# Performance work log

Hardware: AMD Instinct MI355X
Metric: run time of the kernel (lower is better)

Reference implementation:

```python
import jax, jax.numpy as jnp
import numpy as np

B, D, L = 16, 256, 200
T = 1000   # max_frame_length
K = 3      # kernel_size
DW, DC = 4, 2


def setup_inputs() -> dict:
    key = jax.random.key(0)
    ks = jax.random.split(key, 16)
    plen = jax.random.randint(ks[0], (B,), 150, L + 1)
    pm = jnp.arange(L)[None, :] < plen[:, None]              # (B,L) True=valid
    phoneme_mask = pm[:, None, :]                            # (B,1,L)
    durations = jax.random.uniform(ks[1], (B, L), minval=1.0, maxval=8.0) * pm
    phoneme = jax.random.normal(ks[2], (B, D, L), dtype=jnp.float32)
    s = 0.05
    params = {
        'Wpw': jax.random.normal(ks[3], (D, D)) * s, 'bpw': jnp.zeros((D,)),
        'Cw': jax.random.normal(ks[4], (8, D, K)) * s, 'cbw': jnp.zeros((8,)),
        'Mw': jax.random.normal(ks[5], (10, DW)) * s, 'mbw': jnp.zeros((DW,)),
        'Lw': jax.random.normal(ks[6], (DW * D, D)) * s, 'lbw': jnp.zeros((D,)),
        'Wpc': jax.random.normal(ks[7], (D, D)) * s, 'bpc': jnp.zeros((D,)),
        'Cc': jax.random.normal(ks[8], (8, D, K)) * s, 'cbc': jnp.zeros((8,)),
        'Mc': jax.random.normal(ks[9], (10, DC)) * s, 'mbc': jnp.zeros((DC,)),
        'Lc': jax.random.normal(ks[10], (DW * DC, D)) * s, 'lbc': jnp.zeros((D,)),
        'Wo': jax.random.normal(ks[11], (D, 2 * D)) * s, 'bo': jnp.zeros((2 * D,)),
    }
    return {'durations': durations, 'phoneme': phoneme, 'phoneme_mask': phoneme_mask, **params}


def _conv_swish(x, W1, b1, Ck, cb, pm):
    # 1x1 conv (proj) then kernel-K 'same' conv then SiLU; mask padded phones
    h = jnp.einsum('od,bdl->bol', W1, x) + b1[None, :, None]
    h = jax.lax.conv_general_dilated(h, Ck, (1,), 'SAME',
                                     dimension_numbers=('NCH', 'OIH', 'NCH')) + cb[None, :, None]
    h = jax.nn.silu(h)
    h = jnp.where(pm[:, None, :], h, 0.0)
    return h.transpose(0, 2, 1)  # (B, L, 8)


def _mlp(S, E, h, M, mb):
    # concat start/end boundary scalars with per-phone conv features -> (B,T,L,10)
    feat = jnp.concatenate([S[..., None], E[..., None],
                            jnp.broadcast_to(h[:, None], (B, T, L, 8))], axis=-1)
    return jax.nn.silu(feat @ M + mb)


def _forward(durations, phoneme, phoneme_mask, Wpw, bpw, Cw, cbw, Mw, mbw, Lw, lbw,
             Wpc, bpc, Cc, cbc, Mc, mbc, Lc, lbc, Wo, bo):
    pm = phoneme_mask[:, 0, :]                                          # (B,L)
    frame_lengths = jnp.clip(jnp.round(durations.sum(-1)).astype(jnp.int32), 0, T)
    frame_mask = jnp.arange(T)[None, :] < frame_lengths[:, None]        # (B,T)
    attn_mask = frame_mask[:, :, None] & pm[:, None, :]                 # (B,T,L)
    sd = jnp.cumsum(durations, axis=-1)                                 # (B,L)
    sk = sd - durations
    t = jnp.arange(1, T + 1, dtype=durations.dtype)
    S = jnp.where(attn_mask, t[None, :, None] - sk[:, None, :], 0.0)    # (B,T,L)
    E = jnp.where(attn_mask, (sd - sk)[:, None, :], 0.0)                # (B,T,L)

    h_w = _conv_swish(phoneme, Wpw, bpw, Cw, cbw, pm)
    w = _mlp(S, E, h_w, Mw, mbw)                                        # (B,T,L,DW)
    w = jnp.where(pm[:, None, :, None], w, -jnp.inf)
    w = jax.nn.softmax(w, axis=2)                                       # softmax over phones
    w = jnp.where(frame_mask[:, :, None, None], w, 0.0)

    h_c = _conv_swish(phoneme, Wpc, bpc, Cc, cbc, pm)
    c = _mlp(S, E, h_c, Mc, mbc)                                        # (B,T,L,DC)

    wh = jnp.einsum('btlq,bdl->btqd', w, phoneme).reshape(B, T, DW * D) @ Lw + lbw
    wc = jnp.einsum('btlq,btlp->btqp', w, c).reshape(B, T, DW * DC) @ Lc + lbc
    whc = jnp.where(frame_mask[..., None], wh + wc, 0.0)                # (B,T,D)
    out = (whc @ Wo + bo).transpose(0, 2, 1)                            # (B,2D,T)
    return out, frame_mask, frame_lengths, w.transpose(0, 3, 1, 2)


def reference(durations, phoneme, phoneme_mask, Wpw, bpw, Cw, cbw, Mw, mbw, Lw, lbw,
              Wpc, bpc, Cc, cbc, Mc, mbc, Lc, lbc, Wo, bo):
    out, frame_mask, frame_lengths, w = _forward(
        durations, phoneme, phoneme_mask, Wpw, bpw, Cw, cbw, Mw, mbw, Lw, lbw,
        Wpc, bpc, Cc, cbc, Mc, mbc, Lc, lbc, Wo, bo)
    mean, log_std = jnp.split(out, 2, axis=1)                           # (B,D,T) each
    return (mean, log_std, frame_mask, frame_lengths, w)
```

## Files before the change

kernel.cpp:

```cpp
#include <hip/hip_runtime.h>
#include <hip/hip_bf16.h>
#include <math.h>

#define NB 16
#define ND 256
#define NL 200
#define NT 1000

typedef unsigned short ushort_t;
typedef __bf16 bf16x8 __attribute__((ext_vector_type(8)));
typedef float f32x4 __attribute__((ext_vector_type(4)));

#define OFF_PHT   0u
#define OFF_SK    4966400u
#define OFF_EW    4969600u
#define OFF_EC    4975744u
#define OFF_BW2   4981888u
#define OFF_BC2   4981912u
#define OFF_FL    4981936u
#define OFF_GT    11535552u
#define OFF_WHC   13173952u
#define OFF_WOT   15221952u
#define OFF_BASE  15287488u
#define OFF_PHTB  15320256u
#define OFF_LWT   15844544u

__device__ __forceinline__ float silu_f(float x){ return x / (1.f + __expf(-x)); }
__device__ __forceinline__ ushort_t f2bf(float x){
  __hip_bfloat16 h = __float2bfloat16(x);
  return *(ushort_t*)&h;
}

__global__ __launch_bounds__(256) void k_stage1(
    const float* __restrict__ dur, const float* __restrict__ ph,
    const float* __restrict__ Wp_w, const float* __restrict__ C_w, const float* __restrict__ bp_w,
    const float* __restrict__ Wp_c, const float* __restrict__ C_c, const float* __restrict__ bp_c,
    const float* __restrict__ Wo, const float* __restrict__ Lw,
    float* __restrict__ sk_ws, int* __restrict__ fl_ws,
    float* __restrict__ o_fm, float* __restrict__ o_fl,
    float* __restrict__ Ew, float* __restrict__ Ec,
    float* __restrict__ bw2, float* __restrict__ bc2,
    ushort_t* __restrict__ WoT, ushort_t* __restrict__ LwT,
    float* __restrict__ phT, ushort_t* __restrict__ phTb)
{
  int bid = blockIdx.x, tid = threadIdx.x;
  if (bid < 16){
    int b = bid;
    __shared__ float sdur[NL];
    __shared__ float ssk[NL];
    __shared__ int sfl;
    if (tid < NL) sdur[tid] = dur[b*NL + tid];
    __syncthreads();
    if (tid == 0){
      float run = 0.f;
      for (int l = 0; l < NL; ++l){ ssk[l] = run; run += sdur[l]; }
      int fl = (int)rintf(run);
      fl = fl < 0 ? 0 : (fl > NT ? NT : fl);
      sfl = fl; fl_ws[b] = fl; o_fl[b] = (float)fl;
    }
    __syncthreads();
    if (tid < NL) sk_ws[b*NL + tid] = ssk[tid];
    for (int t = tid; t < NT; t += 256) o_fm[b*NT + t] = (t < sfl) ? 1.f : 0.f;
  } else if (bid < 1600){
    int sbid = bid - 16;
    if (sbid < 48){
      int gid = sbid*256 + tid;
      int branch = gid / 6144;
      int r = gid % 6144;
      int d = r & 255;
      int ock = r >> 8;
      int oc = ock / 3, k = ock % 3;
      const float* Wp = branch ? Wp_c : Wp_w;
      const float* C  = branch ? C_c  : C_w;
      float acc = 0.f;
      for (int i = 0; i < ND; ++i) acc += C[(oc*ND + i)*3 + k] * Wp[i*ND + d];
      (branch ? Ec : Ew)[r] = acc;
      if (d == 0){
        const float* bp = branch ? bp_c : bp_w;
        float bb = 0.f;
        for (int i = 0; i < ND; ++i) bb += C[(oc*ND + i)*3 + k] * bp[i];
        (branch ? bc2 : bw2)[ock] = bb;
      }
    } else {
      int gid = (sbid - 48)*256 + tid;
      if (gid < 131072){
        int n = gid >> 8, k = gid & 255;
        WoT[gid] = f2bf(Wo[(size_t)k*512 + n]);
      } else {
        int r = gid - 131072;
        int d = r & 255;
        int qn = r >> 8;
        int q = qn >> 8, n = qn & 255;
        LwT[r] = f2bf(Lw[((size_t)q*256 + d)*256 + n]);
      }
    }
  } else {
    int r = bid - 1600;
    int xb = r & 7, yb = (r >> 3) & 7, b = r >> 6;
    int l0 = xb*32, d0 = yb*32;
    int tx = tid & 31, ty = tid >> 5;
    __shared__ float tile[32][33];
    #pragma unroll
    for (int i = 0; i < 4; ++i){
      int d = d0 + ty + i*8, l = l0 + tx;
      tile[ty + i*8][tx] = (l < NL) ? ph[((size_t)b*ND + d)*NL + l] : 0.f;
    }
    __syncthreads();
    #pragma unroll
    for (int i = 0; i < 4; ++i){
      int l = l0 + ty + i*8, d = d0 + tx;
      float v = tile[tx][ty + i*8];
      if (l < NL) phT[((size_t)b*NL + l)*ND + d] = v;
      phTb[((size_t)b*256 + l)*ND + d] = f2bf(v);
    }
  }
}

__global__ __launch_bounds__(256) void k_stage2(
    const float* __restrict__ phT,
    const float* __restrict__ dur, const float* __restrict__ sk_ws,
    const float* __restrict__ Ew, const float* __restrict__ Ec,
    const float* __restrict__ bw2, const float* __restrict__ bc2,
    const float* __restrict__ cbw, const float* __restrict__ cbc,
    const float* __restrict__ Mw, const float* __restrict__ mbw,
    const float* __restrict__ Mc, const float* __restrict__ mbc,
    float4* __restrict__ base,
    const ushort_t* __restrict__ LwT, const ushort_t* __restrict__ phTb,
    ushort_t* __restrict__ Gt)
{
  __shared__ __align__(16) unsigned char smem[128*136*2];
  int bid = blockIdx.x, tid = threadIdx.x;
  if (bid < 256){
    int b = bid >> 4, x = bid & 15;
    if (x >= 13){
      int l0 = 208 + (x - 13)*16;
      if (tid < 32)
        base[((size_t)(b*256 + l0 + (tid >> 1)))*2 + (tid & 1)] = make_float4(0,0,0,0);
      return;
    }
    float (*sh)[17] = (float (*)[17])smem;
    int lu = tid >> 4, u = tid & 15;
    int l = x*16 + lu;
    float h = 0.f;
    if (l < NL){
      int branch = u >> 3, oc = u & 7;
      const float* E  = branch ? Ec  : Ew;
      const float* b2 = branch ? bc2 : bw2;
      float val = (branch ? cbc : cbw)[oc];
      #pragma unroll
      for (int k = 0; k < 3; ++k){
        int ll = l + k - 1;
        if (ll < 0 || ll >= NL) continue;
        float acc = b2[oc*3 + k];
        const float4* Er = (const float4*)(E + (oc*3 + k)*ND);
        const float4* pr = (const float4*)(phT + ((size_t)b*NL + ll)*ND);
        #pragma unroll 8
        for (int d = 0; d < 64; ++d){
          float4 e = Er[d], p = pr[d];
          acc += e.x*p.x + e.y*p.y + e.z*p.z + e.w*p.w;
        }
        val += acc;
      }
      float pm = (dur[b*NL + l] > 0.5f) ? 1.f : 0.f;
      h = silu_f(val) * pm;
    }
    sh[lu][u] = h;
    __syncthreads();
    if (tid < 16){
      int ll = x*16 + tid;
      float4 o0 = make_float4(0,0,0,0);
      float4 o1 = make_float4(0,0,0,0);
      if (ll < NL){
        float dl  = dur[b*NL + ll];
        float pm  = (dl > 0.5f) ? 1.f : 0.f;
        float skl = sk_ws[b*NL + ll];
        float c1[4], c2[2];
        #pragma unroll
        for (int q = 0; q < 4; ++q) c1[q] = mbw[q] + dl*Mw[4 + q] - skl*Mw[q];
        #pragma unroll
        for (int p = 0; p < 2; ++p) c2[p] = mbc[p] + dl*Mc[2 + p] - skl*Mc[p];
        #pragma unroll
        for (int j = 0; j < 8; ++j){
          float hwv = sh[tid][j], hcv = sh[tid][8 + j];
          #pragma unroll
          for (int q = 0; q < 4; ++q) c1[q] += hwv*Mw[(2 + j)*4 + q];
          #pragma unroll
          for (int p = 0; p < 2; ++p) c2[p] += hcv*Mc[(2 + j)*2 + p];
        }
        o0 = make_float4(c1[0], c1[1], c1[2], c1[3]);
        o1 = make_float4(c2[0], c2[1], pm, 0.f);
      }
      base[((size_t)(b*256 + ll))*2 + 0] = o0;
      base[((size_t)(b*256 + ll))*2 + 1] = o1;
    }
  } else {
    int r = bid - 256;
    int xb = r & 1, yb = (r >> 1) & 1, bq = r >> 2;
    int b = bq >> 2, q = bq & 3;
    int m0 = yb * 128;
    int n0 = xb * 128;
    int lane = tid & 63, wave = tid >> 6;
    int wm = wave >> 1, wn = wave & 1;
    int col = lane & 15, kg4 = lane >> 4;
    f32x4 acc[4][4] = {};
    for (int kt = 0; kt < 8; ++kt){
      int k0 = kt*32;
      bf16x8 afr[4], bfr[4];
      #pragma unroll
      for (int i = 0; i < 4; ++i)
        afr[i] = *(const bf16x8*)(LwT + ((size_t)(q*256 + m0 + wm*64 + i*16 + col))*256 + k0 + kg4*8);
      #pragma unroll
      for (int j = 0; j < 4; ++j)
        bfr[j] = *(const bf16x8*)(phTb + ((size_t)(b*256 + n0 + wn*64 + j*16 + col))*256 + k0 + kg4*8);
      #pragma unroll
      for (int i = 0; i < 4; ++i)
        #pragma unroll
        for (int j = 0; j < 4; ++j)
          acc[i][j] = __builtin_amdgcn_mfma_f32_16x16x32_bf16(afr[i], bfr[j], acc[i][j], 0, 0, 0);
    }
    ushort_t (*st2)[136] = (ushort_t (*)[136])smem;
    int rq = lane >> 4;
    #pragma unroll
    for (int i = 0; i < 4; ++i){
      #pragma unroll
      for (int rr = 0; rr < 4; ++rr){
        int rl = wm*64 + i*16 + rq*4 + rr;
        #pragma unroll
        for (int j = 0; j < 4; ++j){
          int cl = wn*64 + j*16 + col;
          st2[rl][cl] = f2bf(acc[i][j][rr]);
        }
      }
    }
    __syncthreads();
    #pragma unroll
    for (int rep = 0; rep < 8; ++rep){
      int row = rep*16 + (tid >> 4);
      int ch  = tid & 15;
      int l   = n0 + ch*8;
      if (l < NL){
        int n = m0 + row;
        *(uint4*)(Gt + ((size_t)(b*ND + n))*800 + q*NL + l) = *(const uint4*)&st2[row][ch*8];
      }
    }
  }
}

#define AP 808
__global__ __launch_bounds__(256) void k_wv_fused(
    const float4* __restrict__ base,
    const int* __restrict__ fl_ws,
    const float* __restrict__ Mw, const float* __restrict__ Mc,
    const ushort_t* __restrict__ Gt,
    const float* __restrict__ Lc,
    const float* __restrict__ lbc,
    const float* __restrict__ lbw,
    float* __restrict__ wout,
    ushort_t* __restrict__ whc)
{
  __shared__ ushort_t As[32*AP];
  __shared__ float    wcs[32][8];
  int b = blockIdx.y;
  int m0 = blockIdx.x * 32;
  int tid = threadIdx.x, lane = tid & 63, wave = tid >> 6;
  int col = lane & 15, kg4 = lane >> 4;
  int fl = fl_ws[b];

  for (int s = 0; s < 8; ++s){
    int tl = wave*8 + s;
    int t = m0 + tl;
    if (t >= fl){
      for (int k = lane; k < 800; k += 64) As[tl*AP + k] = 0;
      if (lane < 8) wcs[tl][lane] = 0.f;
      if (t < NT){
        float4 z4 = make_float4(0,0,0,0);
        #pragma unroll
        for (int q = 0; q < 4; ++q)
          if (lane < 50)
            *(float4*)&wout[(((size_t)(b*4 + q))*NT + t)*NL + lane*4] = z4;
      }
      continue;
    }
    float t1 = (float)(t + 1);
    float tqw[4], tqc[2];
    #pragma unroll
    for (int q = 0; q < 4; ++q) tqw[q] = t1 * Mw[q];
    #pragma unroll
    for (int p = 0; p < 2; ++p) tqc[p] = t1 * Mc[p];
    float z[4][4], cv[4][2], msk[4];
    float m[4] = {-INFINITY, -INFINITY, -INFINITY, -INFINITY};
    #pragma unroll
    for (int c = 0; c < 4; ++c){
      int l = c*64 + lane;
      float4 b0 = base[((size_t)(b*256 + l))*2 + 0];
      float4 b1 = base[((size_t)(b*256 + l))*2 + 1];
      float pm = b1.z;
      msk[c] = pm;
      float zz[4] = { b0.x + tqw[0], b0.y + tqw[1], b0.z + tqw[2], b0.w + tqw[3] };
      #pragma unroll
      for (int q = 0; q < 4; ++q){
        float sv = silu_f(zz[q]);
        z[c][q] = (pm > 0.f) ? sv : -INFINITY;
        m[q] = fmaxf(m[q], z[c][q]);
      }
      cv[c][0] = silu_f(b1.x + tqc[0]);
      cv[c][1] = silu_f(b1.y + tqc[1]);
    }
    #pragma unroll
    for (int q = 0; q < 4; ++q){
      float v = m[q];
      #pragma unroll
      for (int off = 32; off; off >>= 1) v = fmaxf(v, __shfl_xor(v, off));
      m[q] = v;
    }
    float s4[4] = {0,0,0,0};
    #pragma unroll
    for (int c = 0; c < 4; ++c){
      #pragma unroll
      for (int q = 0; q < 4; ++q){
        float e = (msk[c] > 0.f) ? __expf(z[c][q] - m[q]) : 0.f;
        z[c][q] = e;
        s4[q] += e;
      }
    }
    #pragma unroll
    for (int q = 0; q < 4; ++q){
      float v = s4[q];
      #pragma unroll
      for (int off = 32; off; off >>= 1) v += __shfl_xor(v, off);
      s4[q] = 1.f / v;
    }
    float wc[8] = {0,0,0,0,0,0,0,0};
    #pragma unroll
    for (int c = 0; c < 4; ++c){
      int l = c*64 + lane;
      bool lv = l < NL;
      #pragma unroll
      for (int q = 0; q < 4; ++q){
        float wq = z[c][q] * s4[q];
        if (lv){
          wout[(((size_t)(b*4 + q))*NT + t)*NL + l] = wq;
          As[tl*AP + q*NL + l] = f2bf(wq);
        }
        wc[q*2 + 0] += wq * cv[c][0];
        wc[q*2 + 1] += wq * cv[c][1];
      }
    }
    #pragma unroll
    for (int u = 0; u < 8; ++u){
      float v = wc[u];
      #pragma unroll
      for (int off = 32; off; off >>= 1) v += __shfl_xor(v, off);
      wc[u] = v;
    }
    if (lane == 0){
      #pragma unroll
      for (int u = 0; u < 8; ++u) wcs[tl][u] = wc[u];
    }
  }
  __syncthreads();

  f32x4 acc[2][4] = {};
  const ushort_t* Gb = Gt + (size_t)b*ND*800;
  for (int kt = 0; kt < 25; ++kt){
    int k0 = kt*32;
    bf16x8 afr[2], bfr[4];
    #pragma unroll
    for (int i = 0; i < 2; ++i)
      afr[i] = *(const bf16x8*)(&As[(i*16 + col)*AP + k0 + kg4*8]);
    #pragma unroll
    for (int j = 0; j < 4; ++j)
      bfr[j] = *(const bf16x8*)(Gb + ((size_t)(wave*64 + j*16 + col))*800 + k0 + kg4*8);
    #pragma unroll
    for (int i = 0; i < 2; ++i)
      #pragma unroll
      for (int j = 0; j < 4; ++j)
        acc[i][j] = __builtin_amdgcn_mfma_f32_16x16x32_bf16(afr[i], bfr[j], acc[i][j], 0, 0, 0);
  }
  __syncthreads();

  ushort_t (*stc)[264] = (ushort_t (*)[264])As;
  int rq = lane >> 4;
  float lcn[4][8], lbn[4], lbwn[4];
  #pragma unroll
  for (int j = 0; j < 4; ++j){
    int n = wave*64 + j*16 + col;
    lbn[j] = lbc[n]; lbwn[j] = lbw[n];
    #pragma unroll
    for (int u = 0; u < 8; ++u) lcn[j][u] = Lc[u*ND + n];
  }
  #pragma unroll
  for (int i = 0; i < 2; ++i){
    #pragma unroll
    for (int r = 0; r < 4; ++r){
      int tl = i*16 + rq*4 + r;
      int t = m0 + tl;
      if (t >= NT) continue;
      float f = (t < fl) ? 1.f : 0.f;
      #pragma unroll
      for (int j = 0; j < 4; ++j){
        float vcv = lbn[j]
          + wcs[tl][0]*lcn[j][0] + wcs[tl][1]*lcn[j][1]
          + wcs[tl][2]*lcn[j][2] + wcs[tl][3]*lcn[j][3]
          + wcs[tl][4]*lcn[j][4] + wcs[tl][5]*lcn[j][5]
          + wcs[tl][6]*lcn[j][6] + wcs[tl][7]*lcn[j][7];
        int n = wave*64 + j*16 + col;
        stc[tl][n] = f2bf(f * (acc[i][j][r] + lbwn[j] + vcv));
      }
    }
  }
  __syncthreads();
  #pragma unroll
  for (int rep = 0; rep < 4; ++rep){
    int idx = rep*256 + tid;
    int row = idx >> 5, ch = idx & 31;
    int t = m0 + row;
    if (t < NT)
      *(uint4*)(whc + ((size_t)b*NT + t)*ND + ch*8) = *(const uint4*)&stc[row][ch*8];
  }
}

__global__ __launch_bounds__(256) void k_gemmO_mfma(
    const ushort_t* __restrict__ whc,
    const ushort_t* __restrict__ WoT,
    const float* __restrict__ bo,
    float* __restrict__ o_mean, float* __restrict__ o_lstd)
{
  __shared__ float st[64][132];
  int m0 = blockIdx.y * 128;
  int n0 = blockIdx.x * 128;
  int tid = threadIdx.x, lane = tid & 63, wave = tid >> 6;
  int wm = wave >> 1, wn = wave & 1;
  int col = lane & 15, kg4 = lane >> 4;

  f32x4 acc[4][4] = {};

  for (int kt = 0; kt < 8; ++kt){
    int k0 = kt*32;
    bf16x8 afr[4], bfr[4];
    #pragma unroll
    for (int i = 0; i < 4; ++i)
      afr[i] = *(const bf16x8*)(WoT + ((size_t)(m0 + wm*64 + i*16 + col))*ND + k0 + kg4*8);
    #pragma unroll
    for (int j = 0; j < 4; ++j)
      bfr[j] = *(const bf16x8*)(whc + ((size_t)(n0 + wn*64 + j*16 + col))*ND + k0 + kg4*8);
    #pragma unroll
    for (int i = 0; i < 4; ++i)
      #pragma unroll
      for (int j = 0; j < 4; ++j)
        acc[i][j] = __builtin_amdgcn_mfma_f32_16x16x32_bf16(afr[i], bfr[j], acc[i][j], 0, 0, 0);
  }

  int rq = lane >> 4;
  for (int h = 0; h < 2; ++h){
    if (wm == h){
      #pragma unroll
      for (int i = 0; i < 4; ++i){
        #pragma unroll
        for (int r = 0; r < 4; ++r){
          int rl = i*16 + rq*4 + r;
          #pragma unroll
          for (int j = 0; j < 4; ++j){
            int cl = wn*64 + j*16 + col;
            st[rl][cl] = acc[i][j][r];
          }
        }
      }
    }
    __syncthreads();
    #pragma unroll
    for (int rep = 0; rep < 4; ++rep){
      int row = rep*16 + (tid >> 4);
      int cseg = tid & 15;
      int s = m0 + h*64 + row;
      float bov = bo[s];
      #pragma unroll
      for (int p = 0; p < 2; ++p){
        int c = p*64 + cseg*4;
        int bt = n0 + c;
        int b = bt / NT, t = bt - b*NT;
        float4 v = *(const float4*)&st[row][c];
        v.x += bov; v.y += bov; v.z += bov; v.w += bov;
        if (s < ND) *(float4*)&o_mean[((size_t)b*ND + s)*NT + t] = v;
        else        *(float4*)&o_lstd[((size_t)b*ND + (s - ND))*NT + t] = v;
      }
    }
    __syncthreads();
  }
}

extern "C" void kernel_launch(void* const* d_in, const int* in_sizes, int n_in,
                              void* d_out, int out_size, void* d_ws, size_t ws_size,
                              hipStream_t stream)
{
  const float* dur = (const float*)d_in[0];
  const float* ph  = (const float*)d_in[1];
  const float* Wpw = (const float*)d_in[3];
  const float* bpw = (const float*)d_in[4];
  const float* Cw  = (const float*)d_in[5];
  const float* cbw = (const float*)d_in[6];
  const float* Mw  = (const float*)d_in[7];
  const float* mbw = (const float*)d_in[8];
  const float* Lw  = (const float*)d_in[9];
  const float* lbw = (const float*)d_in[10];
  const float* Wpc = (const float*)d_in[11];
  const float* bpc = (const float*)d_in[12];
  const float* Cc  = (const float*)d_in[13];
  const float* cbc = (const float*)d_in[14];
  const float* Mc  = (const float*)d_in[15];
  const float* mbc = (const float*)d_in[16];
  const float* Lc  = (const float*)d_in[17];
  const float* lbc = (const float*)d_in[18];
  const float* Wo  = (const float*)d_in[19];
  const float* bo  = (const float*)d_in[20];

  float* out    = (float*)d_out;
  float* o_mean = out;
  float* o_lstd = out + (size_t)NB*ND*NT;
  float* o_fm   = o_lstd + (size_t)NB*ND*NT;
  float* o_fl   = o_fm + NB*NT;
  float* o_w    = o_fl + NB;

  float* ws   = (float*)d_ws;
  float* phT  = ws + OFF_PHT;
  float* sk   = ws + OFF_SK;
  float* Ew   = ws + OFF_EW;
  float* Ec   = ws + OFF_EC;
  float* bw2  = ws + OFF_BW2;
  float* bc2  = ws + OFF_BC2;
  int*   fl   = (int*)(ws + OFF_FL);
  ushort_t* Gt   = (ushort_t*)(ws + OFF_GT);
  ushort_t* whc  = (ushort_t*)(ws + OFF_WHC);
  ushort_t* WoT  = (ushort_t*)(ws + OFF_WOT);
  float4*   base = (float4*)(ws + OFF_BASE);
  ushort_t* phTb = (ushort_t*)(ws + OFF_PHTB);
  ushort_t* LwT  = (ushort_t*)(ws + OFF_LWT);

  k_stage1<<<2624, 256, 0, stream>>>(dur, ph, Wpw, Cw, bpw, Wpc, Cc, bpc, Wo, Lw,
                                     sk, fl, o_fm, o_fl, Ew, Ec, bw2, bc2,
                                     WoT, LwT, phT, phTb);
  k_stage2<<<512, 256, 0, stream>>>(phT, dur, sk, Ew, Ec, bw2, bc2, cbw, cbc,
                                    Mw, mbw, Mc, mbc, base, LwT, phTb, Gt);
  {
    dim3 g(32, NB);
    k_wv_fused<<<g, 256, 0, stream>>>(base, fl, Mw, Mc, Gt, Lc, lbc, lbw,
                                      o_w, whc);
  }
  {
    dim3 g(125, 4);
    k_gemmO_mfma<<<g, 256, 0, stream>>>(whc, WoT, bo, o_mean, o_lstd);
  }
}
```

Baseline: 250.6 us.

## Fuse output projection GEMM into wv kernel, drop whc round-trip

```diff
diff --git a/kernel.cpp b/kernel.cpp
--- a/kernel.cpp
+++ b/kernel.cpp
@@ -19,7 +19,6 @@
 #define OFF_BC2   4981912u
 #define OFF_FL    4981936u
 #define OFF_GT    11535552u
-#define OFF_WHC   13173952u
 #define OFF_WOT   15221952u
 #define OFF_BASE  15287488u
 #define OFF_PHTB  15320256u
@@ -255,8 +254,10 @@
     const float* __restrict__ Lc,
     const float* __restrict__ lbc,
     const float* __restrict__ lbw,
+    const ushort_t* __restrict__ WoT,
+    const float* __restrict__ bo,
     float* __restrict__ wout,
-    ushort_t* __restrict__ whc)
+    float* __restrict__ o_mean, float* __restrict__ o_lstd)
 {
   __shared__ ushort_t As[32*AP];
   __shared__ float    wcs[32][8];
@@ -380,112 +381,73 @@
   __syncthreads();
 
   ushort_t (*stc)[264] = (ushort_t (*)[264])As;
-  int rq = lane >> 4;
-  float lcn[4][8], lbn[4], lbwn[4];
-  #pragma unroll
-  for (int j = 0; j < 4; ++j){
-    int n = wave*64 + j*16 + col;
-    lbn[j] = lbc[n]; lbwn[j] = lbw[n];
-    #pragma unroll
-    for (int u = 0; u < 8; ++u) lcn[j][u] = Lc[u*ND + n];
-  }
-  #pragma unroll
-  for (int i = 0; i < 2; ++i){
-    #pragma unroll
-    for (int r = 0; r < 4; ++r){
-      int tl = i*16 + rq*4 + r;
-      int t = m0 + tl;
-      if (t >= NT) continue;
-      float f = (t < fl) ? 1.f : 0.f;
-      #pragma unroll
-      for (int j = 0; j < 4; ++j){
-        float vcv = lbn[j]
-          + wcs[tl][0]*lcn[j][0] + wcs[tl][1]*lcn[j][1]
-          + wcs[tl][2]*lcn[j][2] + wcs[tl][3]*lcn[j][3]
-          + wcs[tl][4]*lcn[j][4] + wcs[tl][5]*lcn[j][5]
-          + wcs[tl][6]*lcn[j][6] + wcs[tl][7]*lcn[j][7];
-        int n = wave*64 + j*16 + col;
-        stc[tl][n] = f2bf(f * (acc[i][j][r] + lbwn[j] + vcv));
+  {
+    int rq = lane >> 4;
+    float lcn[4][8], lbn[4], lbwn[4];
+    #pragma unroll
+    for (int j = 0; j < 4; ++j){
+      int n = wave*64 + j*16 + col;
+      lbn[j] = lbc[n]; lbwn[j] = lbw[n];
+      #pragma unroll
+      for (int u = 0; u < 8; ++u) lcn[j][u] = Lc[u*ND + n];
+    }
+    #pragma unroll
+    for (int i = 0; i < 2; ++i){
+      #pragma unroll
+      for (int r = 0; r < 4; ++r){
+        int tl = i*16 + rq*4 + r;
+        int t = m0 + tl;
+        if (t >= NT) continue;
+        float f = (t < fl) ? 1.f : 0.f;
+        #pragma unroll
+        for (int j = 0; j < 4; ++j){
+          float vcv = lbn[j]
+            + wcs[tl][0]*lcn[j][0] + wcs[tl][1]*lcn[j][1]
+            + wcs[tl][2]*lcn[j][2] + wcs[tl][3]*lcn[j][3]
+            + wcs[tl][4]*lcn[j][4] + wcs[tl][5]*lcn[j][5]
+            + wcs[tl][6]*lcn[j][6] + wcs[tl][7]*lcn[j][7];
+          int n = wave*64 + j*16 + col;
+          stc[tl][n] = f2bf(f * (acc[i][j][r] + lbwn[j] + vcv));
+        }
       }
     }
   }
   __syncthreads();
-  #pragma unroll
-  for (int rep = 0; rep < 4; ++rep){
-    int idx = rep*256 + tid;
-    int row = idx >> 5, ch = idx & 31;
-    int t = m0 + row;
-    if (t < NT)
-      *(uint4*)(whc + ((size_t)b*NT + t)*ND + ch*8) = *(const uint4*)&stc[row][ch*8];
-  }
-}
-
-__global__ __launch_bounds__(256) void k_gemmO_mfma(
-    const ushort_t* __restrict__ whc,
-    const ushort_t* __restrict__ WoT,
-    const float* __restrict__ bo,
-    float* __restrict__ o_mean, float* __restrict__ o_lstd)
-{
-  __shared__ float st[64][132];
-  int m0 = blockIdx.y * 128;
-  int n0 = blockIdx.x * 128;
-  int tid = threadIdx.x, lane = tid & 63, wave = tid >> 6;
-  int wm = wave >> 1, wn = wave & 1;
-  int col = lane & 15, kg4 = lane >> 4;
-
-  f32x4 acc[4][4] = {};
-
-  for (int kt = 0; kt < 8; ++kt){
-    int k0 = kt*32;
-    bf16x8 afr[4], bfr[4];
-    #pragma unroll
-    for (int i = 0; i < 4; ++i)
-      afr[i] = *(const bf16x8*)(WoT + ((size_t)(m0 + wm*64 + i*16 + col))*ND + k0 + kg4*8);
-    #pragma unroll
-    for (int j = 0; j < 4; ++j)
-      bfr[j] = *(const bf16x8*)(whc + ((size_t)(n0 + wn*64 + j*16 + col))*ND + k0 + kg4*8);
-    #pragma unroll
-    for (int i = 0; i < 4; ++i)
-      #pragma unroll
-      for (int j = 0; j < 4; ++j)
-        acc[i][j] = __builtin_amdgcn_mfma_f32_16x16x32_bf16(afr[i], bfr[j], acc[i][j], 0, 0, 0);
-  }
-
-  int rq = lane >> 4;
-  for (int h = 0; h < 2; ++h){
-    if (wm == h){
-      #pragma unroll
-      for (int i = 0; i < 4; ++i){
-        #pragma unroll
-        for (int r = 0; r < 4; ++r){
-          int rl = i*16 + rq*4 + r;
-          #pragma unroll
-          for (int j = 0; j < 4; ++j){
-            int cl = wn*64 + j*16 + col;
-            st[rl][cl] = acc[i][j][r];
-          }
+
+  {
+    f32x4 acc2[8][2] = {};
+    for (int kt = 0; kt < 8; ++kt){
+      int k0 = kt*32;
+      bf16x8 afr[8], bfr[2];
+      #pragma unroll
+      for (int j = 0; j < 2; ++j)
+        bfr[j] = *(const bf16x8*)(&stc[j*16 + col][k0 + kg4*8]);
+      #pragma unroll
+      for (int i = 0; i < 8; ++i)
+        afr[i] = *(const bf16x8*)(WoT + ((size_t)(wave*128 + i*16 + col))*ND + k0 + kg4*8);
+      #pragma unroll
+      for (int i = 0; i < 8; ++i)
+        #pragma unroll
+        for (int j = 0; j < 2; ++j)
+          acc2[i][j] = __builtin_amdgcn_mfma_f32_16x16x32_bf16(afr[i], bfr[j], acc2[i][j], 0, 0, 0);
+    }
+    int rq = lane >> 4;
+    #pragma unroll
+    for (int i = 0; i < 8; ++i){
+      #pragma unroll
+      for (int r = 0; r < 4; ++r){
+        int s = wave*128 + i*16 + rq*4 + r;
+        float bov = bo[s];
+        #pragma unroll
+        for (int j = 0; j < 2; ++j){
+          int t = m0 + j*16 + col;
+          if (t >= NT) continue;
+          float v = acc2[i][j][r] + bov;
+          if (s < ND) o_mean[((size_t)b*ND + s)*NT + t] = v;
+          else        o_lstd[((size_t)b*ND + (s - ND))*NT + t] = v;
         }
       }
     }
-    __syncthreads();
-    #pragma unroll
-    for (int rep = 0; rep < 4; ++rep){
-      int row = rep*16 + (tid >> 4);
-      int cseg = tid & 15;
-      int s = m0 + h*64 + row;
-      float bov = bo[s];
-      #pragma unroll
-      for (int p = 0; p < 2; ++p){
-        int c = p*64 + cseg*4;
-        int bt = n0 + c;
-        int b = bt / NT, t = bt - b*NT;
-        float4 v = *(const float4*)&st[row][c];
-        v.x += bov; v.y += bov; v.z += bov; v.w += bov;
-        if (s < ND) *(float4*)&o_mean[((size_t)b*ND + s)*NT + t] = v;
-        else        *(float4*)&o_lstd[((size_t)b*ND + (s - ND))*NT + t] = v;
-      }
-    }
-    __syncthreads();
   }
 }
 
@@ -530,7 +492,6 @@
   float* bc2  = ws + OFF_BC2;
   int*   fl   = (int*)(ws + OFF_FL);
   ushort_t* Gt   = (ushort_t*)(ws + OFF_GT);
-  ushort_t* whc  = (ushort_t*)(ws + OFF_WHC);
   ushort_t* WoT  = (ushort_t*)(ws + OFF_WOT);
   float4*   base = (float4*)(ws + OFF_BASE);
   ushort_t* phTb = (ushort_t*)(ws + OFF_PHTB);
@@ -544,10 +505,6 @@
   {
     dim3 g(32, NB);
     k_wv_fused<<<g, 256, 0, stream>>>(base, fl, Mw, Mc, Gt, Lc, lbc, lbw,
-                                      o_w, whc);
-  }
-  {
-    dim3 g(125, 4);
-    k_gemmO_mfma<<<g, 256, 0, stream>>>(whc, WoT, bo, o_mean, o_lstd);
+                                      WoT, bo, o_w, o_mean, o_lstd);
   }
 }
```

Result: no change. 247.8 us (-1.1%).
